# Kernel tuning notes

Hardware: AMD Instinct MI355X
Metric: run time of the kernel (lower is better)

Reference implementation:

```python
import jax, jax.numpy as jnp
import numpy as np

HID = 2048   # hidden_size
H = 16       # num_attention_heads
KV = 2       # num_key_value_heads
HD = 256     # head_dim
S = 2048     # seq_len (prefill)
MAX_SEQ = 4096
EPS = 1e-6
RD = HD // 4          # partial RoPE dims (head_dim * 0.25)
SCALE = HD ** (-0.5)
GROUPS = H // KV


def setup_inputs() -> dict:
    key = jax.random.key(0)
    ks = jax.random.split(key, 10)
    hidden_in = jax.random.normal(ks[0], (1, S, HID), jnp.float32)
    ang = jax.random.uniform(ks[1], (1, S, RD), jnp.float32) * (2.0 * np.pi)
    cos = jnp.cos(ang)
    sin = jnp.sin(ang)
    w = 0.02
    q_proj_w = jax.random.normal(ks[2], (2 * H * HD, HID), jnp.float32) * w
    k_proj_w = jax.random.normal(ks[3], (KV * HD, HID), jnp.float32) * w
    v_proj_w = jax.random.normal(ks[4], (KV * HD, HID), jnp.float32) * w
    o_proj_w = jax.random.normal(ks[5], (HID, H * HD), jnp.float32) * w
    q_norm_w = jax.random.normal(ks[6], (HD,), jnp.float32) * 0.1
    k_norm_w = jax.random.normal(ks[7], (HD,), jnp.float32) * 0.1
    return dict(hidden_in=hidden_in, cos=cos, sin=sin,
                q_proj_w=q_proj_w, k_proj_w=k_proj_w, v_proj_w=v_proj_w,
                o_proj_w=o_proj_w, q_norm_w=q_norm_w, k_norm_w=k_norm_w)


def _rmsnorm(x, w):
    var = jnp.mean(x * x, axis=-1, keepdims=True)
    return x * jax.lax.rsqrt(var + EPS) * (1.0 + w)


def _rotate_half(x):
    x1, x2 = jnp.split(x, 2, axis=-1)
    return jnp.concatenate([-x2, x1], axis=-1)


def reference(hidden_in, cos, sin, q_proj_w, k_proj_w, v_proj_w, o_proj_w, q_norm_w, k_norm_w):
    # projections (F.linear => x @ W^T)
    qg = hidden_in @ q_proj_w.T                      # [1, S, 2*H*HD]
    k = hidden_in @ k_proj_w.T                       # [1, S, KV*HD]
    v = hidden_in @ v_proj_w.T

    qg = qg.reshape(1, S, H, 2 * HD)
    q, gate = qg[..., :HD], qg[..., HD:]             # chunk(2, dim=-1)
    gate = gate.reshape(1, S, H * HD)

    q = _rmsnorm(q, q_norm_w).transpose(0, 2, 1, 3)  # [1, H, S, HD]
    k = _rmsnorm(k.reshape(1, S, KV, HD), k_norm_w).transpose(0, 2, 1, 3)  # [1, KV, S, HD]
    v = v.reshape(1, S, KV, HD).transpose(0, 2, 1, 3)                      # [1, KV, S, HD]

    # partial RoPE on first RD dims
    c = cos[:, None, :, :]                           # [1, 1, S, RD]
    s = sin[:, None, :, :]
    q_rot, q_pass = q[..., :RD], q[..., RD:]
    k_rot, k_pass = k[..., :RD], k[..., RD:]
    q = jnp.concatenate([q_rot * c + _rotate_half(q_rot) * s, q_pass], axis=-1)
    k = jnp.concatenate([k_rot * c + _rotate_half(k_rot) * s, k_pass], axis=-1)

    # KV cache padded to max_seq
    zpad = jnp.zeros((1, KV, MAX_SEQ - S, HD), k.dtype)
    k_cache_out = jnp.concatenate([k, zpad], axis=2)
    v_cache_out = jnp.concatenate([v, zpad], axis=2)

    # GQA repeat
    k_r = jnp.repeat(k, GROUPS, axis=1)              # [1, H, S, HD]
    v_r = jnp.repeat(v, GROUPS, axis=1)

    causal = jnp.triu(jnp.full((S, S), -10000.0, jnp.float32), k=1)
    scores = jnp.einsum('bhqd,bhkd->bhqk', q, k_r) * SCALE + causal
    attn_w = jax.nn.softmax(scores, axis=-1)
    attn = jnp.einsum('bhqk,bhkd->bhqd', attn_w, v_r)
    attn = attn.transpose(0, 2, 1, 3).reshape(1, S, H * HD)

    attn = attn * jax.nn.sigmoid(gate)
    hidden_out = attn @ o_proj_w.T                   # [1, S, HID]
    return hidden_out, k_cache_out, v_cache_out
```

## Files before the change

### kernel.cpp

```cpp
#include <hip/hip_runtime.h>

#define S_LEN 2048
#define HID 2048
#define NH 16
#define NKV 2
#define HD 256
#define MAXSEQ 4096
#define NALL 9216
#define RD 64

typedef __attribute__((ext_vector_type(8))) short short8_t;
typedef __attribute__((ext_vector_type(4))) float float4_t;

#define DPPF(x, ctrl) __builtin_bit_cast(float, __builtin_amdgcn_update_dpp( \
    __builtin_bit_cast(int, x), __builtin_bit_cast(int, x), ctrl, 0xF, 0xF, false))

__device__ __forceinline__ unsigned short f2b(float f) {
  union { float f; unsigned u; } v; v.f = f;
  unsigned u = v.u;
  return (unsigned short)((u + 0x7FFFu + ((u >> 16) & 1u)) >> 16);
}

__device__ __forceinline__ void gload_lds16(const void* g, void* l) {
  __builtin_amdgcn_global_load_lds(
      (const __attribute__((address_space(1))) void*)g,
      (__attribute__((address_space(3))) void*)l, 16, 0, 0);
}

__global__ void fused_cvt(const float* __restrict__ hidden, const float* __restrict__ qw,
                          const float* __restrict__ kw, const float* __restrict__ vw,
                          const float* __restrict__ ow,
                          unsigned short* __restrict__ hidb, unsigned short* __restrict__ wallb,
                          unsigned short* __restrict__ wob,
                          float* __restrict__ kcache, float* __restrict__ vcache) {
  const long i = (long)blockIdx.x * 256 + threadIdx.x;
  const long N0 = 1048576, N1 = N0 + 4194304, N2 = N1 + 262144, N3 = N2 + 262144,
             N4 = N3 + 2097152;
  if (i < N4) {
    const float* s; unsigned short* d; long j;
    if (i < N0)      { s = hidden; d = hidb;  j = i; }
    else if (i < N1) { s = qw; d = wallb;                        j = i - N0; }
    else if (i < N2) { s = kw; d = wallb + (size_t)8192*HID;     j = i - N1; }
    else if (i < N3) { s = vw; d = wallb + (size_t)8704*HID;     j = i - N2; }
    else             { s = ow; d = wob;                          j = i - N3; }
    float4 v = ((const float4*)s)[j];
    short4 o;
    o.x = (short)f2b(v.x); o.y = (short)f2b(v.y);
    o.z = (short)f2b(v.z); o.w = (short)f2b(v.w);
    ((short4*)d)[j] = o;
  } else {
    long j = i - N4;
    int region = (int)(j >> 17);
    long o = j & 131071;
    float* base = (region < 2 ? kcache : vcache)
                + (size_t)(region & 1) * MAXSEQ * HD + (size_t)S_LEN * HD;
    float4 z; z.x = 0.f; z.y = 0.f; z.z = 0.f; z.w = 0.f;
    ((float4*)base)[o] = z;
  }
}

template<int BM, int BN, int MI, int NI>
__global__ __launch_bounds__(256, 2) void gemm_bt(
    const unsigned short* __restrict__ A, const unsigned short* __restrict__ B,
    float* __restrict__ C, int M, int N, int K) {
  constexpr int BK = 64;
  __shared__ unsigned short As[BM * BK];
  __shared__ unsigned short Bs[BN * BK];
  const int tid = threadIdx.x;
  const int lane = tid & 63;
  const int w = tid >> 6;
  const int wr = w >> 1, wc = w & 1;
  const int l15 = lane & 15, l4 = lane >> 4;
  const int M0 = blockIdx.y * BM, N0 = blockIdx.x * BN;
  float4_t acc[MI][NI] = {};
  for (int kt = 0; kt < K; kt += BK) {
    __syncthreads();
#pragma unroll
    for (int i = 0; i < BM/32; ++i) {
      int c = tid + i*256;
      int row = c >> 3;
      gload_lds16(A + (size_t)(M0 + row)*K + kt + ((c & 7) ^ (row & 7))*8, (char*)As + c*16);
    }
#pragma unroll
    for (int i = 0; i < BN/32; ++i) {
      int c = tid + i*256;
      int row = c >> 3;
      gload_lds16(B + (size_t)(N0 + row)*K + kt + ((c & 7) ^ (row & 7))*8, (char*)Bs + c*16);
    }
    __syncthreads();
#pragma unroll
    for (int ks = 0; ks < 2; ++ks) {
      short8_t af[MI], bf[NI];
#pragma unroll
      for (int mi = 0; mi < MI; ++mi) {
        int row = wr*(BM/2) + mi*16 + l15;
        af[mi] = *(const short8_t*)&As[row*BK + ((ks*4 + l4) ^ (l15 & 7))*8];
      }
#pragma unroll
      for (int ni = 0; ni < NI; ++ni) {
        int row = wc*(BN/2) + ni*16 + l15;
        bf[ni] = *(const short8_t*)&Bs[row*BK + ((ks*4 + l4) ^ (l15 & 7))*8];
      }
#pragma unroll
      for (int mi = 0; mi < MI; ++mi)
#pragma unroll
        for (int ni = 0; ni < NI; ++ni)
          acc[mi][ni] = __builtin_amdgcn_mfma_f32_16x16x32_bf16(af[mi], bf[ni], acc[mi][ni], 0, 0, 0);
    }
  }
#pragma unroll
  for (int mi = 0; mi < MI; ++mi) {
    int rb = M0 + wr*(BM/2) + mi*16 + l4*4;
#pragma unroll
    for (int ni = 0; ni < NI; ++ni) {
      int col = N0 + wc*(BN/2) + ni*16 + l15;
#pragma unroll
      for (int r = 0; r < 4; ++r)
        C[(size_t)(rb + r)*N + col] = acc[mi][ni][r];
    }
  }
}

__global__ void postproc(const float* __restrict__ C1,
                         const float* __restrict__ cosb, const float* __restrict__ sinb,
                         const float* __restrict__ qnw, const float* __restrict__ knw,
                         unsigned short* __restrict__ qb, unsigned short* __restrict__ kb,
                         unsigned short* __restrict__ vtb,
                         float* __restrict__ kcache, float* __restrict__ vcache) {
  const int w = threadIdx.x >> 6, lane = threadIdx.x & 63;
  const int s = blockIdx.x*4 + w;
  const int t = blockIdx.y;
  const int d = lane*4;
  const float* rowp;
  if (t < 16)      rowp = C1 + (size_t)s*NALL + t*512;
  else if (t < 18) rowp = C1 + (size_t)s*NALL + 8192 + (t-16)*256;
  else             rowp = C1 + (size_t)s*NALL + 8704 + (t-18)*256;
  float4 x = *(const float4*)(rowp + d);
  if (t >= 18) {
    int kvi = t - 18;
    *(float4*)(vcache + (size_t)kvi*MAXSEQ*HD + (size_t)s*HD + d) = x;
    unsigned short* vt = vtb + (size_t)kvi*HD*S_LEN;
    vt[(size_t)(d+0)*S_LEN + s] = f2b(x.x);
    vt[(size_t)(d+1)*S_LEN + s] = f2b(x.y);
    vt[(size_t)(d+2)*S_LEN + s] = f2b(x.z);
    vt[(size_t)(d+3)*S_LEN + s] = f2b(x.w);
    return;
  }
  float ss = x.x*x.x + x.y*x.y + x.z*x.z + x.w*x.w;
#pragma unroll
  for (int o = 32; o >= 1; o >>= 1) ss += __shfl_xor(ss, o, 64);
  float rn = rsqrtf(ss*(1.0f/256.0f) + 1e-6f);
  const float* nw = (t < 16) ? qnw : knw;
  float4 g = *(const float4*)(nw + d);
  float4 y;
  y.x = x.x*rn*(1.f+g.x); y.y = x.y*rn*(1.f+g.y);
  y.z = x.z*rn*(1.f+g.z); y.w = x.w*rn*(1.f+g.w);
  float px = __shfl_xor(y.x, 8, 64);
  float py = __shfl_xor(y.y, 8, 64);
  float pz = __shfl_xor(y.z, 8, 64);
  float pw = __shfl_xor(y.w, 8, 64);
  if (lane < 16) {
    float sgn = (lane & 8) ? 1.f : -1.f;
    float4 cs = *(const float4*)(cosb + (size_t)s*RD + d);
    float4 sn = *(const float4*)(sinb + (size_t)s*RD + d);
    y.x = y.x*cs.x + sgn*px*sn.x;
    y.y = y.y*cs.y + sgn*py*sn.y;
    y.z = y.z*cs.z + sgn*pz*sn.z;
    y.w = y.w*cs.w + sgn*pw*sn.w;
  }
  if (t < 16) {
    const float qs = 0.0625f * 1.44269504088896f;
    short4 o;
    o.x = (short)f2b(y.x*qs); o.y = (short)f2b(y.y*qs);
    o.z = (short)f2b(y.z*qs); o.w = (short)f2b(y.w*qs);
    *(short4*)(qb + (size_t)t*S_LEN*HD + (size_t)s*HD + d) = o;
  } else {
    int kvi = t - 16;
    *(float4*)(kcache + (size_t)kvi*MAXSEQ*HD + (size_t)s*HD + d) = y;
    short4 o;
    o.x = (short)f2b(y.x); o.y = (short)f2b(y.y);
    o.z = (short)f2b(y.z); o.w = (short)f2b(y.w);
    *(short4*)(kb + (size_t)kvi*S_LEN*HD + (size_t)s*HD + d) = o;
  }
}

__global__ __launch_bounds__(512, 2) void attn_kernel(
    const unsigned short* __restrict__ qb, const unsigned short* __restrict__ kb,
    const unsigned short* __restrict__ vtb, const float* __restrict__ C1,
    unsigned short* __restrict__ attnb) {
  __shared__ char smem[73728];
  const int tid = threadIdx.x, lane = tid & 63, w = tid >> 6;
  const int g  = w >> 2;
  const int wq = w & 3;
  const int gtid = tid & 255;
  const int l15 = lane & 15, l4 = lane >> 4;
  unsigned short* Ks  = (unsigned short*)(smem + g*16384);
  unsigned short* VTs = (unsigned short*)(smem + 32768 + g*16384);
  unsigned short* Pw  = (unsigned short*)(smem + 65536 + w*1024);
  const int b = blockIdx.x;
  const int i2 = b & 255;
  const int h = i2 & 15;
  const int t16 = i2 >> 4;
  const int qt = (b < 256) ? t16 : (31 - t16);
  const int kv = h >> 3;
  const int q0 = qt * 64;
  const unsigned short* Qb = qb + (size_t)h*S_LEN*HD;
  const unsigned short* Kb = kb + (size_t)kv*S_LEN*HD;
  const unsigned short* Vb = vtb + (size_t)kv*HD*S_LEN;
  const int qrow = q0 + wq*16 + l15;
  short8_t qf[8];
#pragma unroll
  for (int kk = 0; kk < 8; ++kk)
    qf[kk] = *(const short8_t*)(Qb + (size_t)qrow*HD + kk*32 + l4*8);
  float4_t oacc[16] = {};
  float m_run[4] = {-1e30f, -1e30f, -1e30f, -1e30f};
  float l_run[4] = {0.f, 0.f, 0.f, 0.f};
  const int nIt = qt + 1;
  const int tbase = g * nIt;
  for (int it = 0; it < nIt; ++it) {
    const int tIdx = tbase + it;
    const int k0 = tIdx * 32;
    __syncthreads();
#pragma unroll
    for (int i = 0; i < 4; ++i) {
      int c = gtid + i*256;
      int row = c >> 5;
      gload_lds16(Kb + (size_t)(k0 + row)*HD + ((c & 31) ^ (row & 7))*8, (char*)Ks + c*16);
    }
#pragma unroll
    for (int i = 0; i < 4; ++i) {
      int c = gtid + i*256;
      int row = c >> 2;
      gload_lds16(Vb + (size_t)row*S_LEN + k0 + ((c & 3) ^ ((row >> 1) & 3))*8, (char*)VTs + c*16);
    }
    asm volatile("s_waitcnt vmcnt(4)" ::: "memory");
    __builtin_amdgcn_s_barrier();
    __builtin_amdgcn_sched_barrier(0);
    float4_t sacc[2] = {};
#pragma unroll
    for (int nt = 0; nt < 2; ++nt)
#pragma unroll
      for (int kk = 0; kk < 8; ++kk) {
        short8_t bfr = *(const short8_t*)&Ks[(nt*16 + l15)*HD + ((kk*4 + l4) ^ (l15 & 7))*8];
        sacc[nt] = __builtin_amdgcn_mfma_f32_16x16x32_bf16(qf[kk], bfr, sacc[nt], 0, 0, 0);
      }
    if (tIdx >= 2*qt) {
#pragma unroll
      for (int nt = 0; nt < 2; ++nt)
#pragma unroll
        for (int r = 0; r < 4; ++r)
          if (k0 + nt*16 + l15 > q0 + wq*16 + l4*4 + r) sacc[nt][r] = -1e30f;
    }
    float m0[4], p[2][4];
#pragma unroll
    for (int r = 0; r < 4; ++r) {
      float v = fmaxf(sacc[0][r], sacc[1][r]);
      v = fmaxf(v, DPPF(v, 0xB1));
      v = fmaxf(v, DPPF(v, 0x4E));
      v = fmaxf(v, DPPF(v, 0x141));
      v = fmaxf(v, DPPF(v, 0x140));
      m0[r] = v;
    }
    int need = (m0[0] > m_run[0] + 4.f) | (m0[1] > m_run[1] + 4.f) |
               (m0[2] > m_run[2] + 4.f) | (m0[3] > m_run[3] + 4.f);
    if (__any(need)) {
      float al[4];
#pragma unroll
      for (int r = 0; r < 4; ++r) {
        float mnew = fmaxf(m_run[r], m0[r]);
        al[r] = exp2f(m_run[r] - mnew);
        m_run[r] = mnew;
        l_run[r] *= al[r];
      }
#pragma unroll
      for (int nt2 = 0; nt2 < 16; ++nt2) {
        oacc[nt2][0] *= al[0];
        oacc[nt2][1] *= al[1];
        oacc[nt2][2] *= al[2];
        oacc[nt2][3] *= al[3];
      }
    }
#pragma unroll
    for (int r = 0; r < 4; ++r) {
      p[0][r] = exp2f(sacc[0][r] - m_run[r]);
      p[1][r] = exp2f(sacc[1][r] - m_run[r]);
      float sum = p[0][r] + p[1][r];
      sum += DPPF(sum, 0xB1);
      sum += DPPF(sum, 0x4E);
      sum += DPPF(sum, 0x141);
      sum += DPPF(sum, 0x140);
      l_run[r] += sum;
    }
#pragma unroll
    for (int nt = 0; nt < 2; ++nt)
#pragma unroll
      for (int r = 0; r < 4; ++r) {
        int prow = l4*4 + r;
        int pcol = nt*16 + l15;
        Pw[prow*32 + (((pcol >> 3) ^ ((prow >> 1) & 3)))*8 + (pcol & 7)] = f2b(p[nt][r]);
      }
    short8_t pf = *(const short8_t*)&Pw[l15*32 + ((l4 ^ ((l15 >> 1) & 3)))*8];
    __syncthreads();
#pragma unroll
    for (int nt2 = 0; nt2 < 16; ++nt2) {
      int vrow = nt2*16 + l15;
      short8_t v0 = *(const short8_t*)&VTs[vrow*32 + ((l4 ^ ((vrow >> 1) & 3)))*8];
      oacc[nt2] = __builtin_amdgcn_mfma_f32_16x16x32_bf16(pf, v0, oacc[nt2], 0, 0, 0);
    }
  }
  __syncthreads();
  float* Od = (float*)smem;
  float* ML = (float*)(smem + 69632);
  const int r0 = wq*16 + l4*4;
  if (g == 1) {
#pragma unroll
    for (int r = 0; r < 4; ++r)
      if (l15 == 0) { ML[(r0 + r)*2] = m_run[r]; ML[(r0 + r)*2 + 1] = l_run[r]; }
#pragma unroll
    for (int nt2 = 0; nt2 < 16; ++nt2) {
      int dim = nt2*16 + l15;
#pragma unroll
      for (int r = 0; r < 4; ++r)
        Od[(r0 + r)*258 + dim] = oacc[nt2][r];
    }
  }
  __syncthreads();
  if (g == 0) {
    float fA[4], fB[4], inv_l[4];
#pragma unroll
    for (int r = 0; r < 4; ++r) {
      float mB = ML[(r0 + r)*2];
      float lB = ML[(r0 + r)*2 + 1];
      float m = fmaxf(m_run[r], mB);
      fA[r] = exp2f(m_run[r] - m);
      fB[r] = exp2f(mB - m);
      inv_l[r] = 1.f / (l_run[r]*fA[r] + lB*fB[r]);
    }
    const int srow0 = q0 + wq*16 + l4*4;
#pragma unroll
    for (int nt2 = 0; nt2 < 16; ++nt2) {
      int dim = nt2*16 + l15;
#pragma unroll
      for (int r = 0; r < 4; ++r) {
        int srow = srow0 + r;
        float ov = oacc[nt2][r]*fA[r] + Od[(r0 + r)*258 + dim]*fB[r];
        float gv = C1[(size_t)srow*NALL + h*512 + 256 + dim];
        float sg = 1.f / (1.f + __expf(-gv));
        attnb[(size_t)srow*(NH*HD) + h*HD + dim] = f2b(ov * inv_l[r] * sg);
      }
    }
  }
}

extern "C" void kernel_launch(void* const* d_in, const int* in_sizes, int n_in,
                              void* d_out, int out_size, void* d_ws, size_t ws_size,
                              hipStream_t stream) {
  const float* hidden = (const float*)d_in[0];
  const float* cosb   = (const float*)d_in[1];
  const float* sinb   = (const float*)d_in[2];
  const float* qw     = (const float*)d_in[3];
  const float* kw     = (const float*)d_in[4];
  const float* vw     = (const float*)d_in[5];
  const float* ow     = (const float*)d_in[6];
  const float* qnw    = (const float*)d_in[7];
  const float* knw    = (const float*)d_in[8];
  float* out    = (float*)d_out;
  float* kcache = out + (size_t)S_LEN*HID;
  float* vcache = kcache + (size_t)NKV*MAXSEQ*HD;

  char* ws = (char*)d_ws;
  size_t off = 0;
  auto alloc = [&](size_t bytes) -> char* {
    char* p = ws + off; off += (bytes + 255) & ~(size_t)255; return p;
  };
  unsigned short* hidb  = (unsigned short*)alloc((size_t)S_LEN*HID*2);
  unsigned short* wallb = (unsigned short*)alloc((size_t)NALL*HID*2);
  unsigned short* wob   = (unsigned short*)alloc((size_t)HID*NH*HD*2);
  float*          C1    = (float*)alloc((size_t)S_LEN*NALL*4);
  unsigned short* qb    = (unsigned short*)alloc((size_t)NH*S_LEN*HD*2);
  unsigned short* kb    = (unsigned short*)alloc((size_t)NKV*S_LEN*HD*2);
  unsigned short* vtb   = (unsigned short*)alloc((size_t)NKV*HD*S_LEN*2);
  unsigned short* attnb = (unsigned short*)alloc((size_t)S_LEN*NH*HD*2);

  fused_cvt<<<32768, 256, 0, stream>>>(hidden, qw, kw, vw, ow,
                                       hidb, wallb, wob, kcache, vcache);

  gemm_bt<128,128,4,4><<<dim3(NALL/128, S_LEN/128), 256, 0, stream>>>(
      hidb, wallb, C1, S_LEN, NALL, HID);

  postproc<<<dim3(S_LEN/4, 20), 256, 0, stream>>>(
      C1, cosb, sinb, qnw, knw, qb, kb, vtb, kcache, vcache);

  attn_kernel<<<512, 512, 0, stream>>>(qb, kb, vtb, C1, attnb);

  gemm_bt<128,128,4,4><<<dim3(HID/128, S_LEN/128), 256, 0, stream>>>(
      attnb, wob, out, S_LEN, HID, NH*HD);
}
```

Measured before the change: 451.2 us.

## Give each attention wave two query fragments and halve block threads; retile output GEMM

```diff
diff --git a/kernel.cpp b/kernel.cpp
--- a/kernel.cpp
+++ b/kernel.cpp
@@ -184,19 +184,19 @@
   }
 }
 
-__global__ __launch_bounds__(512, 2) void attn_kernel(
+__global__ __launch_bounds__(256, 2) void attn_kernel(
     const unsigned short* __restrict__ qb, const unsigned short* __restrict__ kb,
     const unsigned short* __restrict__ vtb, const float* __restrict__ C1,
     unsigned short* __restrict__ attnb) {
   __shared__ char smem[73728];
   const int tid = threadIdx.x, lane = tid & 63, w = tid >> 6;
-  const int g  = w >> 2;
-  const int wq = w & 3;
-  const int gtid = tid & 255;
+  const int g  = w >> 1;
+  const int wv = w & 1;
+  const int gtid = tid & 127;
   const int l15 = lane & 15, l4 = lane >> 4;
   unsigned short* Ks  = (unsigned short*)(smem + g*16384);
   unsigned short* VTs = (unsigned short*)(smem + 32768 + g*16384);
-  unsigned short* Pw  = (unsigned short*)(smem + 65536 + w*1024);
+  unsigned short* Pw  = (unsigned short*)(smem + 65536 + w*2048);
   const int b = blockIdx.x;
   const int i2 = b & 255;
   const int h = i2 & 15;
@@ -207,14 +207,17 @@
   const unsigned short* Qb = qb + (size_t)h*S_LEN*HD;
   const unsigned short* Kb = kb + (size_t)kv*S_LEN*HD;
   const unsigned short* Vb = vtb + (size_t)kv*HD*S_LEN;
-  const int qrow = q0 + wq*16 + l15;
-  short8_t qf[8];
-#pragma unroll
-  for (int kk = 0; kk < 8; ++kk)
-    qf[kk] = *(const short8_t*)(Qb + (size_t)qrow*HD + kk*32 + l4*8);
-  float4_t oacc[16] = {};
-  float m_run[4] = {-1e30f, -1e30f, -1e30f, -1e30f};
-  float l_run[4] = {0.f, 0.f, 0.f, 0.f};
+  short8_t qf[2][8];
+#pragma unroll
+  for (int fr = 0; fr < 2; ++fr) {
+    const int qrow = q0 + wv*32 + fr*16 + l15;
+#pragma unroll
+    for (int kk = 0; kk < 8; ++kk)
+      qf[fr][kk] = *(const short8_t*)(Qb + (size_t)qrow*HD + kk*32 + l4*8);
+  }
+  float4_t oacc[2][16] = {};
+  float m_run[2][4] = {{-1e30f,-1e30f,-1e30f,-1e30f},{-1e30f,-1e30f,-1e30f,-1e30f}};
+  float l_run[2][4] = {};
   const int nIt = qt + 1;
   const int tbase = g * nIt;
   for (int it = 0; it < nIt; ++it) {
@@ -222,131 +225,157 @@
     const int k0 = tIdx * 32;
     __syncthreads();
 #pragma unroll
-    for (int i = 0; i < 4; ++i) {
-      int c = gtid + i*256;
+    for (int i = 0; i < 8; ++i) {
+      int c = gtid + i*128;
       int row = c >> 5;
       gload_lds16(Kb + (size_t)(k0 + row)*HD + ((c & 31) ^ (row & 7))*8, (char*)Ks + c*16);
     }
 #pragma unroll
-    for (int i = 0; i < 4; ++i) {
-      int c = gtid + i*256;
+    for (int i = 0; i < 8; ++i) {
+      int c = gtid + i*128;
       int row = c >> 2;
       gload_lds16(Vb + (size_t)row*S_LEN + k0 + ((c & 3) ^ ((row >> 1) & 3))*8, (char*)VTs + c*16);
     }
-    asm volatile("s_waitcnt vmcnt(4)" ::: "memory");
+    asm volatile("s_waitcnt vmcnt(8)" ::: "memory");
     __builtin_amdgcn_s_barrier();
     __builtin_amdgcn_sched_barrier(0);
-    float4_t sacc[2] = {};
-#pragma unroll
-    for (int nt = 0; nt < 2; ++nt)
-#pragma unroll
-      for (int kk = 0; kk < 8; ++kk) {
-        short8_t bfr = *(const short8_t*)&Ks[(nt*16 + l15)*HD + ((kk*4 + l4) ^ (l15 & 7))*8];
-        sacc[nt] = __builtin_amdgcn_mfma_f32_16x16x32_bf16(qf[kk], bfr, sacc[nt], 0, 0, 0);
-      }
+    float4_t sacc[2][2] = {};
+#pragma unroll
+    for (int kk = 0; kk < 8; ++kk) {
+      short8_t b0 = *(const short8_t*)&Ks[(l15)*HD      + ((kk*4 + l4) ^ (l15 & 7))*8];
+      short8_t b1 = *(const short8_t*)&Ks[(16 + l15)*HD + ((kk*4 + l4) ^ (l15 & 7))*8];
+      sacc[0][0] = __builtin_amdgcn_mfma_f32_16x16x32_bf16(qf[0][kk], b0, sacc[0][0], 0, 0, 0);
+      sacc[0][1] = __builtin_amdgcn_mfma_f32_16x16x32_bf16(qf[0][kk], b1, sacc[0][1], 0, 0, 0);
+      sacc[1][0] = __builtin_amdgcn_mfma_f32_16x16x32_bf16(qf[1][kk], b0, sacc[1][0], 0, 0, 0);
+      sacc[1][1] = __builtin_amdgcn_mfma_f32_16x16x32_bf16(qf[1][kk], b1, sacc[1][1], 0, 0, 0);
+    }
     if (tIdx >= 2*qt) {
 #pragma unroll
+      for (int fr = 0; fr < 2; ++fr)
+#pragma unroll
+        for (int nt = 0; nt < 2; ++nt)
+#pragma unroll
+          for (int r = 0; r < 4; ++r)
+            if (k0 + nt*16 + l15 > q0 + wv*32 + fr*16 + l4*4 + r) sacc[fr][nt][r] = -1e30f;
+    }
+    float m0[2][4], p[2][2][4];
+#pragma unroll
+    for (int fr = 0; fr < 2; ++fr)
+#pragma unroll
+      for (int r = 0; r < 4; ++r) {
+        float v = fmaxf(sacc[fr][0][r], sacc[fr][1][r]);
+        v = fmaxf(v, DPPF(v, 0xB1));
+        v = fmaxf(v, DPPF(v, 0x4E));
+        v = fmaxf(v, DPPF(v, 0x141));
+        v = fmaxf(v, DPPF(v, 0x140));
+        m0[fr][r] = v;
+      }
+    int need = 0;
+#pragma unroll
+    for (int fr = 0; fr < 2; ++fr)
+#pragma unroll
+      for (int r = 0; r < 4; ++r)
+        need |= (m0[fr][r] > m_run[fr][r] + 4.f);
+    if (__any(need)) {
+#pragma unroll
+      for (int fr = 0; fr < 2; ++fr) {
+        float al[4];
+#pragma unroll
+        for (int r = 0; r < 4; ++r) {
+          float mnew = fmaxf(m_run[fr][r], m0[fr][r]);
+          al[r] = exp2f(m_run[fr][r] - mnew);
+          m_run[fr][r] = mnew;
+          l_run[fr][r] *= al[r];
+        }
+#pragma unroll
+        for (int nt2 = 0; nt2 < 16; ++nt2) {
+          oacc[fr][nt2][0] *= al[0];
+          oacc[fr][nt2][1] *= al[1];
+          oacc[fr][nt2][2] *= al[2];
+          oacc[fr][nt2][3] *= al[3];
+        }
+      }
+    }
+#pragma unroll
+    for (int fr = 0; fr < 2; ++fr)
+#pragma unroll
+      for (int r = 0; r < 4; ++r) {
+        p[fr][0][r] = exp2f(sacc[fr][0][r] - m_run[fr][r]);
+        p[fr][1][r] = exp2f(sacc[fr][1][r] - m_run[fr][r]);
+        float sum = p[fr][0][r] + p[fr][1][r];
+        sum += DPPF(sum, 0xB1);
+        sum += DPPF(sum, 0x4E);
+        sum += DPPF(sum, 0x141);
+        sum += DPPF(sum, 0x140);
+        l_run[fr][r] += sum;
+      }
+#pragma unroll
+    for (int fr = 0; fr < 2; ++fr)
+#pragma unroll
       for (int nt = 0; nt < 2; ++nt)
 #pragma unroll
-        for (int r = 0; r < 4; ++r)
-          if (k0 + nt*16 + l15 > q0 + wq*16 + l4*4 + r) sacc[nt][r] = -1e30f;
-    }
-    float m0[4], p[2][4];
-#pragma unroll
-    for (int r = 0; r < 4; ++r) {
-      float v = fmaxf(sacc[0][r], sacc[1][r]);
-      v = fmaxf(v, DPPF(v, 0xB1));
-      v = fmaxf(v, DPPF(v, 0x4E));
-      v = fmaxf(v, DPPF(v, 0x141));
-      v = fmaxf(v, DPPF(v, 0x140));
-      m0[r] = v;
-    }
-    int need = (m0[0] > m_run[0] + 4.f) | (m0[1] > m_run[1] + 4.f) |
-               (m0[2] > m_run[2] + 4.f) | (m0[3] > m_run[3] + 4.f);
-    if (__any(need)) {
-      float al[4];
-#pragma unroll
-      for (int r = 0; r < 4; ++r) {
-        float mnew = fmaxf(m_run[r], m0[r]);
-        al[r] = exp2f(m_run[r] - mnew);
-        m_run[r] = mnew;
-        l_run[r] *= al[r];
-      }
-#pragma unroll
-      for (int nt2 = 0; nt2 < 16; ++nt2) {
-        oacc[nt2][0] *= al[0];
-        oacc[nt2][1] *= al[1];
-        oacc[nt2][2] *= al[2];
-        oacc[nt2][3] *= al[3];
-      }
-    }
-#pragma unroll
-    for (int r = 0; r < 4; ++r) {
-      p[0][r] = exp2f(sacc[0][r] - m_run[r]);
-      p[1][r] = exp2f(sacc[1][r] - m_run[r]);
-      float sum = p[0][r] + p[1][r];
-      sum += DPPF(sum, 0xB1);
-      sum += DPPF(sum, 0x4E);
-      sum += DPPF(sum, 0x141);
-      sum += DPPF(sum, 0x140);
-      l_run[r] += sum;
-    }
-#pragma unroll
-    for (int nt = 0; nt < 2; ++nt)
-#pragma unroll
-      for (int r = 0; r < 4; ++r) {
-        int prow = l4*4 + r;
-        int pcol = nt*16 + l15;
-        Pw[prow*32 + (((pcol >> 3) ^ ((prow >> 1) & 3)))*8 + (pcol & 7)] = f2b(p[nt][r]);
-      }
-    short8_t pf = *(const short8_t*)&Pw[l15*32 + ((l4 ^ ((l15 >> 1) & 3)))*8];
+        for (int r = 0; r < 4; ++r) {
+          int prow = fr*16 + l4*4 + r;
+          int pcol = nt*16 + l15;
+          Pw[prow*32 + (((pcol >> 3) ^ ((prow >> 1) & 3)))*8 + (pcol & 7)] = f2b(p[fr][nt][r]);
+        }
+    short8_t pf0 = *(const short8_t*)&Pw[(l15)*32      + ((l4 ^ ((l15 >> 1) & 3)))*8];
+    short8_t pf1 = *(const short8_t*)&Pw[(16 + l15)*32 + ((l4 ^ (((16 + l15) >> 1) & 3)))*8];
     __syncthreads();
 #pragma unroll
     for (int nt2 = 0; nt2 < 16; ++nt2) {
       int vrow = nt2*16 + l15;
       short8_t v0 = *(const short8_t*)&VTs[vrow*32 + ((l4 ^ ((vrow >> 1) & 3)))*8];
-      oacc[nt2] = __builtin_amdgcn_mfma_f32_16x16x32_bf16(pf, v0, oacc[nt2], 0, 0, 0);
+      oacc[0][nt2] = __builtin_amdgcn_mfma_f32_16x16x32_bf16(pf0, v0, oacc[0][nt2], 0, 0, 0);
+      oacc[1][nt2] = __builtin_amdgcn_mfma_f32_16x16x32_bf16(pf1, v0, oacc[1][nt2], 0, 0, 0);
     }
   }
   __syncthreads();
   float* Od = (float*)smem;
   float* ML = (float*)(smem + 69632);
-  const int r0 = wq*16 + l4*4;
   if (g == 1) {
 #pragma unroll
-    for (int r = 0; r < 4; ++r)
-      if (l15 == 0) { ML[(r0 + r)*2] = m_run[r]; ML[(r0 + r)*2 + 1] = l_run[r]; }
-#pragma unroll
-    for (int nt2 = 0; nt2 < 16; ++nt2) {
-      int dim = nt2*16 + l15;
+    for (int fr = 0; fr < 2; ++fr) {
+      const int r0 = wv*32 + fr*16 + l4*4;
 #pragma unroll
       for (int r = 0; r < 4; ++r)
-        Od[(r0 + r)*258 + dim] = oacc[nt2][r];
+        if (l15 == 0) { ML[(r0 + r)*2] = m_run[fr][r]; ML[(r0 + r)*2 + 1] = l_run[fr][r]; }
+#pragma unroll
+      for (int nt2 = 0; nt2 < 16; ++nt2) {
+        int dim = nt2*16 + l15;
+#pragma unroll
+        for (int r = 0; r < 4; ++r)
+          Od[(r0 + r)*258 + dim] = oacc[fr][nt2][r];
+      }
     }
   }
   __syncthreads();
   if (g == 0) {
-    float fA[4], fB[4], inv_l[4];
-#pragma unroll
-    for (int r = 0; r < 4; ++r) {
-      float mB = ML[(r0 + r)*2];
-      float lB = ML[(r0 + r)*2 + 1];
-      float m = fmaxf(m_run[r], mB);
-      fA[r] = exp2f(m_run[r] - m);
-      fB[r] = exp2f(mB - m);
-      inv_l[r] = 1.f / (l_run[r]*fA[r] + lB*fB[r]);
-    }
-    const int srow0 = q0 + wq*16 + l4*4;
-#pragma unroll
-    for (int nt2 = 0; nt2 < 16; ++nt2) {
-      int dim = nt2*16 + l15;
+#pragma unroll
+    for (int fr = 0; fr < 2; ++fr) {
+      const int r0 = wv*32 + fr*16 + l4*4;
+      float fA[4], fB[4], inv_l[4];
 #pragma unroll
       for (int r = 0; r < 4; ++r) {
-        int srow = srow0 + r;
-        float ov = oacc[nt2][r]*fA[r] + Od[(r0 + r)*258 + dim]*fB[r];
-        float gv = C1[(size_t)srow*NALL + h*512 + 256 + dim];
-        float sg = 1.f / (1.f + __expf(-gv));
-        attnb[(size_t)srow*(NH*HD) + h*HD + dim] = f2b(ov * inv_l[r] * sg);
+        float mB = ML[(r0 + r)*2];
+        float lB = ML[(r0 + r)*2 + 1];
+        float m = fmaxf(m_run[fr][r], mB);
+        fA[r] = exp2f(m_run[fr][r] - m);
+        fB[r] = exp2f(mB - m);
+        inv_l[r] = 1.f / (l_run[fr][r]*fA[r] + lB*fB[r]);
+      }
+      const int srow0 = q0 + r0;
+#pragma unroll
+      for (int nt2 = 0; nt2 < 16; ++nt2) {
+        int dim = nt2*16 + l15;
+#pragma unroll
+        for (int r = 0; r < 4; ++r) {
+          int srow = srow0 + r;
+          float ov = oacc[fr][nt2][r]*fA[r] + Od[(r0 + r)*258 + dim]*fB[r];
+          float gv = C1[(size_t)srow*NALL + h*512 + 256 + dim];
+          float sg = 1.f / (1.f + __expf(-gv));
+          attnb[(size_t)srow*(NH*HD) + h*HD + dim] = f2b(ov * inv_l[r] * sg);
+        }
       }
     }
   }
@@ -391,8 +420,8 @@
   postproc<<<dim3(S_LEN/4, 20), 256, 0, stream>>>(
       C1, cosb, sinb, qnw, knw, qb, kb, vtb, kcache, vcache);
 
-  attn_kernel<<<512, 512, 0, stream>>>(qb, kb, vtb, C1, attnb);
-
-  gemm_bt<128,128,4,4><<<dim3(HID/128, S_LEN/128), 256, 0, stream>>>(
+  attn_kernel<<<512, 256, 0, stream>>>(qb, kb, vtb, C1, attnb);
+
+  gemm_bt<128,64,4,2><<<dim3(HID/64, S_LEN/128), 256, 0, stream>>>(
       attnb, wob, out, S_LEN, HID, NH*HD);
 }
```

Result: slower. 676.4 us (+49.9%).

## Restructure attention into paired q-tile phases with shared 64-key tiles

Applied to the files above, without the earlier changes.

```diff
diff --git a/kernel.cpp b/kernel.cpp
--- a/kernel.cpp
+++ b/kernel.cpp
@@ -192,161 +192,161 @@
   const int tid = threadIdx.x, lane = tid & 63, w = tid >> 6;
   const int g  = w >> 2;
   const int wq = w & 3;
-  const int gtid = tid & 255;
   const int l15 = lane & 15, l4 = lane >> 4;
-  unsigned short* Ks  = (unsigned short*)(smem + g*16384);
-  unsigned short* VTs = (unsigned short*)(smem + 32768 + g*16384);
+  unsigned short* Ks  = (unsigned short*)smem;
+  unsigned short* VTs = (unsigned short*)(smem + 32768);
   unsigned short* Pw  = (unsigned short*)(smem + 65536 + w*1024);
   const int b = blockIdx.x;
-  const int i2 = b & 255;
-  const int h = i2 & 15;
-  const int t16 = i2 >> 4;
-  const int qt = (b < 256) ? t16 : (31 - t16);
+  const int h = b & 15;
+  const int pi = b >> 4;
   const int kv = h >> 3;
-  const int q0 = qt * 64;
   const unsigned short* Qb = qb + (size_t)h*S_LEN*HD;
   const unsigned short* Kb = kb + (size_t)kv*S_LEN*HD;
   const unsigned short* Vb = vtb + (size_t)kv*HD*S_LEN;
-  const int qrow = q0 + wq*16 + l15;
-  short8_t qf[8];
-#pragma unroll
-  for (int kk = 0; kk < 8; ++kk)
-    qf[kk] = *(const short8_t*)(Qb + (size_t)qrow*HD + kk*32 + l4*8);
-  float4_t oacc[16] = {};
-  float m_run[4] = {-1e30f, -1e30f, -1e30f, -1e30f};
-  float l_run[4] = {0.f, 0.f, 0.f, 0.f};
-  const int nIt = qt + 1;
-  const int tbase = g * nIt;
-  for (int it = 0; it < nIt; ++it) {
-    const int tIdx = tbase + it;
-    const int k0 = tIdx * 32;
+  for (int ph = 0; ph < 2; ++ph) {
+    const int qt = ph ? (31 - pi) : pi;
+    const int q0 = qt * 64;
+    const int qrow = q0 + wq*16 + l15;
+    short8_t qf[8];
+#pragma unroll
+    for (int kk = 0; kk < 8; ++kk)
+      qf[kk] = *(const short8_t*)(Qb + (size_t)qrow*HD + kk*32 + l4*8);
+    float4_t oacc[16] = {};
+    float m_run[4] = {-1e29f, -1e29f, -1e29f, -1e29f};
+    float l_run[4] = {0.f, 0.f, 0.f, 0.f};
+    const int nT = qt + 1;
+    for (int t = 0; t < nT; ++t) {
+      const int k0 = t * 64;
+      __syncthreads();
+#pragma unroll
+      for (int i = 0; i < 4; ++i) {
+        int c = tid + i*512;
+        int row = c >> 5;
+        gload_lds16(Kb + (size_t)(k0 + row)*HD + ((c & 31) ^ (row & 7))*8, (char*)Ks + c*16);
+      }
+#pragma unroll
+      for (int i = 0; i < 4; ++i) {
+        int c = tid + i*512;
+        int row = c >> 3;
+        gload_lds16(Vb + (size_t)row*S_LEN + k0 + ((c & 7) ^ (row & 7))*8,
+                    (char*)VTs + c*16);
+      }
+      asm volatile("s_waitcnt vmcnt(4)" ::: "memory");
+      __builtin_amdgcn_s_barrier();
+      __builtin_amdgcn_sched_barrier(0);
+      float4_t sacc[2] = {};
+#pragma unroll
+      for (int nt = 0; nt < 2; ++nt)
+#pragma unroll
+        for (int kk = 0; kk < 8; ++kk) {
+          int krow = g*32 + nt*16 + l15;
+          short8_t bfr = *(const short8_t*)&Ks[krow*HD + ((kk*4 + l4) ^ (l15 & 7))*8];
+          sacc[nt] = __builtin_amdgcn_mfma_f32_16x16x32_bf16(qf[kk], bfr, sacc[nt], 0, 0, 0);
+        }
+      if (t == qt) {
+#pragma unroll
+        for (int nt = 0; nt < 2; ++nt)
+#pragma unroll
+          for (int r = 0; r < 4; ++r)
+            if (k0 + g*32 + nt*16 + l15 > q0 + wq*16 + l4*4 + r) sacc[nt][r] = -1e30f;
+      }
+      float m0[4], p[2][4];
+#pragma unroll
+      for (int r = 0; r < 4; ++r) {
+        float v = fmaxf(sacc[0][r], sacc[1][r]);
+        v = fmaxf(v, DPPF(v, 0xB1));
+        v = fmaxf(v, DPPF(v, 0x4E));
+        v = fmaxf(v, DPPF(v, 0x141));
+        v = fmaxf(v, DPPF(v, 0x140));
+        m0[r] = v;
+      }
+      int need = (m0[0] > m_run[0] + 4.f) | (m0[1] > m_run[1] + 4.f) |
+                 (m0[2] > m_run[2] + 4.f) | (m0[3] > m_run[3] + 4.f);
+      if (__any(need)) {
+        float al[4];
+#pragma unroll
+        for (int r = 0; r < 4; ++r) {
+          float mnew = fmaxf(m_run[r], m0[r]);
+          al[r] = exp2f(m_run[r] - mnew);
+          m_run[r] = mnew;
+          l_run[r] *= al[r];
+        }
+#pragma unroll
+        for (int nt2 = 0; nt2 < 16; ++nt2) {
+          oacc[nt2][0] *= al[0];
+          oacc[nt2][1] *= al[1];
+          oacc[nt2][2] *= al[2];
+          oacc[nt2][3] *= al[3];
+        }
+      }
+#pragma unroll
+      for (int r = 0; r < 4; ++r) {
+        p[0][r] = exp2f(sacc[0][r] - m_run[r]);
+        p[1][r] = exp2f(sacc[1][r] - m_run[r]);
+        float sum = p[0][r] + p[1][r];
+        sum += DPPF(sum, 0xB1);
+        sum += DPPF(sum, 0x4E);
+        sum += DPPF(sum, 0x141);
+        sum += DPPF(sum, 0x140);
+        l_run[r] += sum;
+      }
+#pragma unroll
+      for (int nt = 0; nt < 2; ++nt)
+#pragma unroll
+        for (int r = 0; r < 4; ++r) {
+          int prow = l4*4 + r;
+          int pcol = nt*16 + l15;
+          Pw[prow*32 + (((pcol >> 3) ^ ((prow >> 1) & 3)))*8 + (pcol & 7)] = f2b(p[nt][r]);
+        }
+      short8_t pf = *(const short8_t*)&Pw[l15*32 + ((l4 ^ ((l15 >> 1) & 3)))*8];
+      __syncthreads();
+#pragma unroll
+      for (int nt2 = 0; nt2 < 16; ++nt2) {
+        int vrow = nt2*16 + l15;
+        short8_t v0 = *(const short8_t*)&VTs[vrow*64 + ((4*g + l4) ^ (vrow & 7))*8];
+        oacc[nt2] = __builtin_amdgcn_mfma_f32_16x16x32_bf16(pf, v0, oacc[nt2], 0, 0, 0);
+      }
+    }
     __syncthreads();
-#pragma unroll
-    for (int i = 0; i < 4; ++i) {
-      int c = gtid + i*256;
-      int row = c >> 5;
-      gload_lds16(Kb + (size_t)(k0 + row)*HD + ((c & 31) ^ (row & 7))*8, (char*)Ks + c*16);
-    }
-#pragma unroll
-    for (int i = 0; i < 4; ++i) {
-      int c = gtid + i*256;
-      int row = c >> 2;
-      gload_lds16(Vb + (size_t)row*S_LEN + k0 + ((c & 3) ^ ((row >> 1) & 3))*8, (char*)VTs + c*16);
-    }
-    asm volatile("s_waitcnt vmcnt(4)" ::: "memory");
-    __builtin_amdgcn_s_barrier();
-    __builtin_amdgcn_sched_barrier(0);
-    float4_t sacc[2] = {};
-#pragma unroll
-    for (int nt = 0; nt < 2; ++nt)
-#pragma unroll
-      for (int kk = 0; kk < 8; ++kk) {
-        short8_t bfr = *(const short8_t*)&Ks[(nt*16 + l15)*HD + ((kk*4 + l4) ^ (l15 & 7))*8];
-        sacc[nt] = __builtin_amdgcn_mfma_f32_16x16x32_bf16(qf[kk], bfr, sacc[nt], 0, 0, 0);
-      }
-    if (tIdx >= 2*qt) {
-#pragma unroll
-      for (int nt = 0; nt < 2; ++nt)
+    float* Od = (float*)smem;
+    float* ML = (float*)(smem + 69632);
+    const int r0 = wq*16 + l4*4;
+    if (g == 1) {
+#pragma unroll
+      for (int r = 0; r < 4; ++r)
+        if (l15 == 0) { ML[(r0 + r)*2] = m_run[r]; ML[(r0 + r)*2 + 1] = l_run[r]; }
+#pragma unroll
+      for (int nt2 = 0; nt2 < 16; ++nt2) {
+        int dim = nt2*16 + l15;
 #pragma unroll
         for (int r = 0; r < 4; ++r)
-          if (k0 + nt*16 + l15 > q0 + wq*16 + l4*4 + r) sacc[nt][r] = -1e30f;
-    }
-    float m0[4], p[2][4];
-#pragma unroll
-    for (int r = 0; r < 4; ++r) {
-      float v = fmaxf(sacc[0][r], sacc[1][r]);
-      v = fmaxf(v, DPPF(v, 0xB1));
-      v = fmaxf(v, DPPF(v, 0x4E));
-      v = fmaxf(v, DPPF(v, 0x141));
-      v = fmaxf(v, DPPF(v, 0x140));
-      m0[r] = v;
-    }
-    int need = (m0[0] > m_run[0] + 4.f) | (m0[1] > m_run[1] + 4.f) |
-               (m0[2] > m_run[2] + 4.f) | (m0[3] > m_run[3] + 4.f);
-    if (__any(need)) {
-      float al[4];
+          Od[(r0 + r)*258 + dim] = oacc[nt2][r];
+      }
+    }
+    __syncthreads();
+    if (g == 0) {
+      float fA[4], fB[4], inv_l[4];
 #pragma unroll
       for (int r = 0; r < 4; ++r) {
-        float mnew = fmaxf(m_run[r], m0[r]);
-        al[r] = exp2f(m_run[r] - mnew);
-        m_run[r] = mnew;
-        l_run[r] *= al[r];
-      }
+        float mB = ML[(r0 + r)*2];
+        float lB = ML[(r0 + r)*2 + 1];
+        float m = fmaxf(m_run[r], mB);
+        fA[r] = exp2f(m_run[r] - m);
+        fB[r] = exp2f(mB - m);
+        inv_l[r] = 1.f / (l_run[r]*fA[r] + lB*fB[r]);
+      }
+      const int srow0 = q0 + r0;
 #pragma unroll
       for (int nt2 = 0; nt2 < 16; ++nt2) {
-        oacc[nt2][0] *= al[0];
-        oacc[nt2][1] *= al[1];
-        oacc[nt2][2] *= al[2];
-        oacc[nt2][3] *= al[3];
-      }
-    }
-#pragma unroll
-    for (int r = 0; r < 4; ++r) {
-      p[0][r] = exp2f(sacc[0][r] - m_run[r]);
-      p[1][r] = exp2f(sacc[1][r] - m_run[r]);
-      float sum = p[0][r] + p[1][r];
-      sum += DPPF(sum, 0xB1);
-      sum += DPPF(sum, 0x4E);
-      sum += DPPF(sum, 0x141);
-      sum += DPPF(sum, 0x140);
-      l_run[r] += sum;
-    }
-#pragma unroll
-    for (int nt = 0; nt < 2; ++nt)
-#pragma unroll
-      for (int r = 0; r < 4; ++r) {
-        int prow = l4*4 + r;
-        int pcol = nt*16 + l15;
-        Pw[prow*32 + (((pcol >> 3) ^ ((prow >> 1) & 3)))*8 + (pcol & 7)] = f2b(p[nt][r]);
-      }
-    short8_t pf = *(const short8_t*)&Pw[l15*32 + ((l4 ^ ((l15 >> 1) & 3)))*8];
-    __syncthreads();
-#pragma unroll
-    for (int nt2 = 0; nt2 < 16; ++nt2) {
-      int vrow = nt2*16 + l15;
-      short8_t v0 = *(const short8_t*)&VTs[vrow*32 + ((l4 ^ ((vrow >> 1) & 3)))*8];
-      oacc[nt2] = __builtin_amdgcn_mfma_f32_16x16x32_bf16(pf, v0, oacc[nt2], 0, 0, 0);
-    }
-  }
-  __syncthreads();
-  float* Od = (float*)smem;
-  float* ML = (float*)(smem + 69632);
-  const int r0 = wq*16 + l4*4;
-  if (g == 1) {
-#pragma unroll
-    for (int r = 0; r < 4; ++r)
-      if (l15 == 0) { ML[(r0 + r)*2] = m_run[r]; ML[(r0 + r)*2 + 1] = l_run[r]; }
-#pragma unroll
-    for (int nt2 = 0; nt2 < 16; ++nt2) {
-      int dim = nt2*16 + l15;
-#pragma unroll
-      for (int r = 0; r < 4; ++r)
-        Od[(r0 + r)*258 + dim] = oacc[nt2][r];
-    }
-  }
-  __syncthreads();
-  if (g == 0) {
-    float fA[4], fB[4], inv_l[4];
-#pragma unroll
-    for (int r = 0; r < 4; ++r) {
-      float mB = ML[(r0 + r)*2];
-      float lB = ML[(r0 + r)*2 + 1];
-      float m = fmaxf(m_run[r], mB);
-      fA[r] = exp2f(m_run[r] - m);
-      fB[r] = exp2f(mB - m);
-      inv_l[r] = 1.f / (l_run[r]*fA[r] + lB*fB[r]);
-    }
-    const int srow0 = q0 + wq*16 + l4*4;
-#pragma unroll
-    for (int nt2 = 0; nt2 < 16; ++nt2) {
-      int dim = nt2*16 + l15;
-#pragma unroll
-      for (int r = 0; r < 4; ++r) {
-        int srow = srow0 + r;
-        float ov = oacc[nt2][r]*fA[r] + Od[(r0 + r)*258 + dim]*fB[r];
-        float gv = C1[(size_t)srow*NALL + h*512 + 256 + dim];
-        float sg = 1.f / (1.f + __expf(-gv));
-        attnb[(size_t)srow*(NH*HD) + h*HD + dim] = f2b(ov * inv_l[r] * sg);
+        int dim = nt2*16 + l15;
+#pragma unroll
+        for (int r = 0; r < 4; ++r) {
+          int srow = srow0 + r;
+          float ov = oacc[nt2][r]*fA[r] + Od[(r0 + r)*258 + dim]*fB[r];
+          float gv = C1[(size_t)srow*NALL + h*512 + 256 + dim];
+          float sg = 1.f / (1.f + __expf(-gv));
+          attnb[(size_t)srow*(NH*HD) + h*HD + dim] = f2b(ov * inv_l[r] * sg);
+        }
       }
     }
   }
@@ -391,8 +391,8 @@
   postproc<<<dim3(S_LEN/4, 20), 256, 0, stream>>>(
       C1, cosb, sinb, qnw, knw, qb, kb, vtb, kcache, vcache);
 
-  attn_kernel<<<512, 512, 0, stream>>>(qb, kb, vtb, C1, attnb);
-
-  gemm_bt<128,128,4,4><<<dim3(HID/128, S_LEN/128), 256, 0, stream>>>(
+  attn_kernel<<<256, 512, 0, stream>>>(qb, kb, vtb, C1, attnb);
+
+  gemm_bt<128,64,4,2><<<dim3(HID/64, S_LEN/128), 256, 0, stream>>>(
       attnb, wob, out, S_LEN, HID, NH*HD);
 }
```

After: 421.8 us. 1.07x faster.
